# Kernel optimization log

Measured on AMD Instinct MI355X. Metric: run time of the kernel, lower is better.

## Reference

```python
import jax, jax.numpy as jnp
import numpy as np

N_NODES = 100000
N_EDGES = 2000000
FEAT = 4
H = 64
L = 3  # num_mp_layers
E = 2  # edge_types


def _p(key, shape, scale=0.05):
    return jax.random.normal(key, shape, dtype=jnp.float32) * scale


def setup_inputs() -> dict:
    key = jax.random.key(0)
    ks = jax.random.split(key, 24)
    inp = {
        "x": jax.random.normal(ks[0], (N_NODES, FEAT), dtype=jnp.float32),
        "node_type": jax.random.randint(ks[1], (N_NODES,), 0, 3),
        "edge_index": jax.random.randint(ks[2], (2, N_EDGES), 0, N_NODES),
        "edge_type": jax.random.randint(ks[3], (N_EDGES,), 0, E),
        # input_proj: Linear(4,64) + LayerNorm(64)
        "in_w": _p(ks[4], (FEAT, H)), "in_b": _p(ks[5], (H,)),
        "ln_g": jnp.ones((H,), jnp.float32), "ln_b": jnp.zeros((H,), jnp.float32),
        # per-layer, per-edge-type message MLPs: Linear(2H,H) -> ReLU -> Linear(H,H)
        "mlp_w1": _p(ks[6], (L, E, 2 * H, H)), "mlp_b1": _p(ks[7], (L, E, H)),
        "mlp_w2": _p(ks[8], (L, E, H, H)), "mlp_b2": _p(ks[9], (L, E, H)),
        # per-layer GRUCell(H,H): gates ordered [r, z, n] as in torch
        "gru_wi": _p(ks[10], (L, H, 3 * H)), "gru_wh": _p(ks[11], (L, H, 3 * H)),
        "gru_bi": _p(ks[12], (L, 3 * H)), "gru_bh": _p(ks[13], (L, 3 * H)),
        # readout: Linear(H,H) -> ReLU -> Linear(H,1)
        "ro_w1": _p(ks[14], (H, H)), "ro_b1": _p(ks[15], (H,)),
        "ro_w2": _p(ks[16], (H, 1)), "ro_b2": _p(ks[17], (1,)),
    }
    return inp


def _layernorm(h, g, b, eps=1e-5):
    mu = jnp.mean(h, axis=-1, keepdims=True)
    var = jnp.mean(jnp.square(h - mu), axis=-1, keepdims=True)
    return (h - mu) * jax.lax.rsqrt(var + eps) * g + b


def _forward(x, edge_index, edge_type, node_type,
             in_w, in_b, ln_g, ln_b,
             mlp_w1, mlp_b1, mlp_w2, mlp_b2,
             gru_wi, gru_wh, gru_bi, gru_bh,
             ro_w1, ro_b1, ro_w2, ro_b2):
    n = x.shape[0]
    # input projection (dropout is identity at inference)
    h = jax.nn.relu(_layernorm(x @ in_w + in_b, ln_g, ln_b))
    src, dst = edge_index[0], edge_index[1]
    for l in range(L):
        # gather -> concat: (M, 2H)
        mi = jnp.concatenate([h[src], h[dst]], axis=1)
        msg = jnp.zeros((mi.shape[0], H), dtype=h.dtype)
        for e in range(E):
            m = jax.nn.relu(mi @ mlp_w1[l, e] + mlp_b1[l, e]) @ mlp_w2[l, e] + mlp_b2[l, e]
            msg = msg + jnp.where((edge_type == e)[:, None], m, jnp.zeros((), h.dtype))
        # scatter_add over destination nodes
        agg = jax.ops.segment_sum(msg, dst, num_segments=n)
        # GRUCell(agg, h), torch gate order [r, z, n]
        gi = agg @ gru_wi[l] + gru_bi[l]
        gh = h @ gru_wh[l] + gru_bh[l]
        i_r, i_z, i_n = jnp.split(gi, 3, axis=-1)
        h_r, h_z, h_n = jnp.split(gh, 3, axis=-1)
        r = jax.nn.sigmoid(i_r + h_r)
        z = jax.nn.sigmoid(i_z + h_z)
        nn_ = jnp.tanh(i_n + r * h_n)
        h = (1.0 - z) * nn_ + z * h
    out = jax.nn.relu(h @ ro_w1 + ro_b1) @ ro_w2 + ro_b2  # (N, 1)
    # additive correction for data qubits (node_type==0); other nodes zeroed
    corr = jnp.where(node_type == 0, x[:, 0] + out[:, 0], jnp.zeros((), x.dtype))
    return corr


def reference(x, node_type, edge_index, edge_type,
              in_w, in_b, ln_g, ln_b,
              mlp_w1, mlp_b1, mlp_w2, mlp_b2,
              gru_wi, gru_wh, gru_bi, gru_bh,
              ro_w1, ro_b1, ro_w2, ro_b2):
    return _forward(x, edge_index, edge_type, node_type,
                    in_w, in_b, ln_g, ln_b,
                    mlp_w1, mlp_b1, mlp_w2, mlp_b2,
                    gru_wi, gru_wh, gru_bi, gru_bh,
                    ro_w1, ro_b1, ro_w2, ro_b2)
```

## Files before the change

kernel.cpp:

```cpp
#include <hip/hip_runtime.h>

typedef unsigned int u32;
typedef unsigned short u16;
typedef unsigned long long u64;

using short8 = __attribute__((ext_vector_type(8))) short;
using f32x4  = __attribute__((ext_vector_type(4))) float;

__device__ __forceinline__ u32 f2bf(float f) {
    u32 u = __float_as_uint(f);
    return (u + 0x7fffu + ((u >> 16) & 1u)) >> 16;
}
__device__ __forceinline__ u32 pk(float a, float b) {
    return f2bf(a) | (f2bf(b) << 16);
}
__device__ __forceinline__ u32 f2bf_fast(float f) {
    return (__float_as_uint(f) + 0x8000u) >> 16;
}
__device__ __forceinline__ u32 pk_fast(float a, float b) {
    return f2bf_fast(a) | (f2bf_fast(b) << 16);
}
__device__ __forceinline__ float bflo(u32 u) { return __uint_as_float(u << 16); }
__device__ __forceinline__ float bfhi(u32 u) { return __uint_as_float(u & 0xffff0000u); }
__device__ __forceinline__ float bfu(u16 u) { return __uint_as_float(((u32)u) << 16); }

union U8 { u32 u[4]; short8 v; };

__global__ void k_input_proj(const float* __restrict__ x, const float* __restrict__ in_w,
                             const float* __restrict__ in_b, const float* __restrict__ ln_g,
                             const float* __restrict__ ln_b, u16* __restrict__ hbf, int n_nodes) {
    const int lane = threadIdx.x & 63;
    const int node = blockIdx.x * 4 + (threadIdx.x >> 6);
    if (node >= n_nodes) return;
    float acc = in_b[lane];
#pragma unroll
    for (int k = 0; k < 4; ++k) acc = fmaf(x[node * 4 + k], in_w[k * 64 + lane], acc);
    float s = acc;
#pragma unroll
    for (int off = 32; off > 0; off >>= 1) s += __shfl_xor(s, off);
    float mu = s * (1.f / 64.f);
    float d = acc - mu;
    float vs = d * d;
#pragma unroll
    for (int off = 32; off > 0; off >>= 1) vs += __shfl_xor(vs, off);
    float inv = rsqrtf(vs * (1.f / 64.f) + 1e-5f);
    float hv = fmaxf(d * inv * ln_g[lane] + ln_b[lane], 0.f);
    hbf[(size_t)node * 64 + lane] = (u16)f2bf(hv);
}

__global__ void k_hist(const int* __restrict__ dst, const int* __restrict__ ety,
                       int* __restrict__ cnt, int M, int N) {
    int i = blockIdx.x * 256 + threadIdx.x;
    if (i < M) atomicAdd(&cnt[(ety[i] & 1) * N + dst[i]], 1);
}

__global__ void k_scan1(int* __restrict__ data, int* __restrict__ part, int N) {
    __shared__ int s[1024];
    const int t = threadIdx.x;
    const int i = blockIdx.x * 1024 + t;
    int v = (i < N) ? data[i] : 0;
    s[t] = v;
    __syncthreads();
#pragma unroll
    for (int d = 1; d < 1024; d <<= 1) {
        int x = (t >= d) ? s[t - d] : 0;
        __syncthreads();
        s[t] += x;
        __syncthreads();
    }
    if (i < N) data[i] = s[t] - v;
    if (t == 1023) part[blockIdx.x] = s[1023];
}

__global__ void k_scan2(int* __restrict__ part, int nb) {
    const int l = threadIdx.x & 63;
    int base = 0;
    for (int s = 0; s < nb; s += 64) {
        int i = s + l;
        int orig = (i < nb) ? part[i] : 0;
        int x = orig;
#pragma unroll
        for (int off = 1; off < 64; off <<= 1) {
            int t = __shfl_up(x, off);
            if (l >= off) x += t;
        }
        if (i < nb) part[i] = base + x - orig;
        base += __shfl(x, 63);
    }
}

__global__ void k_scan3(int* __restrict__ data, const int* __restrict__ part, int N,
                        int saveIdx, int* __restrict__ slot) {
    int i = blockIdx.x * 1024 + threadIdx.x;
    if (i < N) {
        int v = data[i] + part[blockIdx.x];
        data[i] = v;
        if (i == saveIdx) slot[0] = v;
    }
}

__global__ void k_filldst(const int* __restrict__ off, int* __restrict__ dstP,
                          int NB, int N, int M) {
    int b = blockIdx.x * 256 + threadIdx.x;
    if (b >= NB) return;
    int s = off[b];
    int e = (b + 1 < NB) ? off[b + 1] : M;
    int d = (b >= N) ? b - N : b;
    for (int p = s; p < e; ++p) dstP[p] = d;
}

__global__ void k_scatter(const int* __restrict__ src, const int* __restrict__ dst,
                          const int* __restrict__ ety, int* __restrict__ cursor,
                          int* __restrict__ srcP, int M, int N, int nd8) {
    const int g = blockIdx.x & 7;
    const int nb = gridDim.x >> 3;
    const int bi = blockIdx.x >> 3;
    for (int e = bi * 256 + threadIdx.x; e < M; e += nb * 256) {
        int d = dst[e];
        if (d / nd8 == g) {
            int t = ety[e] & 1;
            int pos = atomicAdd(&cursor[t * N + d], 1);
            srcP[pos] = src[e] & 0x3FFFFFFF;
        }
    }
}

__global__ __launch_bounds__(256, 2) void k_edge_mlp(
    const u16* __restrict__ hbf, const int* __restrict__ srcP, const int* __restrict__ dstP,
    const int* __restrict__ t0p, const float* __restrict__ w1, const float* __restrict__ b1,
    const float* __restrict__ w2, const float* __restrict__ b2,
    float* __restrict__ agg, int M) {
    __shared__ u16 sHid[4][4608];
    __shared__ u16 sMsg[4][4864];

    const int tid = threadIdx.x;
    const int l = tid & 63, wv = tid >> 6;
    const int l15 = l & 15, quad = l >> 4;
    const f32x4 vz = {0.f, 0.f, 0.f, 0.f};

    const int T0 = *t0p;
    const int half = gridDim.x >> 1;
    const int ty = (blockIdx.x >= half) ? 1 : 0;
    const int bi = ty ? (int)blockIdx.x - half : (int)blockIdx.x;

    const int n_tiles = (M + 63) >> 6;
    const int tlo = ty ? (T0 >> 6) : 0;
    const int thi = ty ? n_tiles : ((T0 + 63) >> 6);
    const int lo = ty ? T0 : 0;
    const int hi = ty ? M : T0;
    const int range = thi - tlo;
    const int per = (range + half - 1) / half;
    const int c0 = tlo + bi * per;
    const int c1 = min(c0 + per, thi);

    short8 Bf1[4][4], Bf2[2][4];
    float b1r[4], b2r[4];
#pragma unroll
    for (int ni = 0; ni < 4; ++ni) {
        const int c = ni * 16 + l15;
        b1r[ni] = b1[ty * 64 + c];
        b2r[ni] = b2[ty * 64 + c];
#pragma unroll
        for (int s = 0; s < 4; ++s) {
            U8 tmp;
            const float* wp = w1 + (size_t)ty * 8192 + (size_t)(s * 32 + quad * 8) * 64 + c;
#pragma unroll
            for (int jp = 0; jp < 4; ++jp) tmp.u[jp] = pk(wp[(2 * jp) * 64], wp[(2 * jp + 1) * 64]);
            Bf1[s][ni] = tmp.v;
        }
#pragma unroll
        for (int s = 0; s < 2; ++s) {
            U8 tmp;
            const float* wp = w2 + (size_t)ty * 4096 + (size_t)(s * 32 + quad * 8) * 64 + c;
#pragma unroll
            for (int jp = 0; jp < 4; ++jp) tmp.u[jp] = pk(wp[(2 * jp) * 64], wp[(2 * jp + 1) * 64]);
            Bf2[s][ni] = tmp.v;
        }
    }

    u16* hid = sHid[wv];
    u16* msg = sMsg[wv];

    int t = c0 + wv;
    int mdc = -1;
    int msn = 0, mdn = -1;
    short8 a1[4][4];
    if (t < c1) {
        int ec = min((t << 6) + l, M - 1);
        int ms = srcP[ec];
        mdc = dstP[ec];
#pragma unroll
        for (int mi = 0; mi < 4; ++mi) {
            int rs = __shfl(ms, mi * 16 + l15);
            int rd = __shfl(mdc, mi * 16 + l15);
#pragma unroll
            for (int s = 0; s < 4; ++s) {
                const int row = (s < 2) ? rs : rd;
                a1[mi][s] = *(const short8*)(hbf + (size_t)row * 64 + (s & 1) * 32 + quad * 8);
            }
        }
        int ecn = min(((t + 4) << 6) + l, M - 1);
        msn = srcP[ecn];
        mdn = dstP[ecn];
    }

    for (; t < c1; t += 4) {
        const int base = t << 6;
        const int ecf = min(((t + 8) << 6) + l, M - 1);
        const int msf = srcP[ecf];
        const int mdf = dstP[ecf];

#pragma unroll
        for (int mi = 0; mi < 4; ++mi) {
            f32x4 acc[4] = {vz, vz, vz, vz};
#pragma unroll
            for (int s = 0; s < 4; ++s)
#pragma unroll
                for (int ni = 0; ni < 4; ++ni)
                    acc[ni] = __builtin_amdgcn_mfma_f32_16x16x32_bf16(a1[mi][s], Bf1[s][ni], acc[ni], 0, 0, 0);
            {
                int rs = __shfl(msn, mi * 16 + l15);
                int rd = __shfl(mdn, mi * 16 + l15);
#pragma unroll
                for (int s = 0; s < 4; ++s) {
                    const int row = (s < 2) ? rs : rd;
                    a1[mi][s] = *(const short8*)(hbf + (size_t)row * 64 + (s & 1) * 32 + quad * 8);
                }
            }
#pragma unroll
            for (int ni = 0; ni < 4; ++ni) {
                const int c = ni * 16 + l15;
#pragma unroll
                for (int r = 0; r < 4; ++r) {
                    float hv = fmaxf(acc[ni][r] + b1r[ni], 0.f);
                    hid[(mi * 16 + quad * 4 + r) * 72 + c] = (u16)f2bf_fast(hv);
                }
            }
        }

#pragma unroll
        for (int mi = 0; mi < 4; ++mi) {
            short8 a2a = *(const short8*)(hid + (mi * 16 + l15) * 72 + quad * 8);
            short8 a2b = *(const short8*)(hid + (mi * 16 + l15) * 72 + 32 + quad * 8);
#pragma unroll
            for (int ni = 0; ni < 4; ++ni) {
                f32x4 tt = __builtin_amdgcn_mfma_f32_16x16x32_bf16(a2a, Bf2[0][ni], vz, 0, 0, 0);
                f32x4 m2 = __builtin_amdgcn_mfma_f32_16x16x32_bf16(a2b, Bf2[1][ni], tt, 0, 0, 0);
                const int c = ni * 16 + l15;
                const int e0 = mi * 16 + quad * 4;
                const float bb = b2r[ni];
                uint2 w;
                w.x = pk_fast(m2[0] + bb, m2[1] + bb);
                w.y = pk_fast(m2[2] + bb, m2[3] + bb);
                *(uint2*)(msg + c * 76 + e0) = w;
            }
        }

        {
            int eg = base + l;
            int dvz = (eg >= lo && eg < hi) ? mdc : -1;
            int dprev = __shfl_up(dvz, 1);
            u64 mask = __ballot((l == 0) || (dvz != dprev));
            float a = 0.f;
#pragma unroll
            for (int i = 0; i < 64; i += 4) {
                uint2 pr = *(const uint2*)(msg + l * 76 + i);
                float v0 = bflo(pr.x), v1 = bfhi(pr.x), v2 = bflo(pr.y), v3 = bfhi(pr.y);
#define RR_STEP(ii, vv)                                                         \
                a += (vv);                                                      \
                if ((ii) == 63 || ((mask >> ((ii) + 1)) & 1ull)) {              \
                    int dd = __builtin_amdgcn_readlane(dvz, (ii));              \
                    if (dd >= 0) unsafeAtomicAdd(agg + (size_t)dd * 64 + l, a); \
                    a = 0.f;                                                    \
                }
                RR_STEP(i, v0)
                RR_STEP(i + 1, v1)
                RR_STEP(i + 2, v2)
                RR_STEP(i + 3, v3)
#undef RR_STEP
            }
        }
        mdc = mdn;
        msn = msf;
        mdn = mdf;
    }
}

__global__ __launch_bounds__(256, 2) void k_gru_gemm(
    float* __restrict__ agg, u16* __restrict__ hbf,
    const float* __restrict__ wi, const float* __restrict__ wh,
    const float* __restrict__ bi, const float* __restrict__ bh, int n_nodes) {
    extern __shared__ u16 smem[];
    u16* sRZ = smem;
    u16* sIN = smem + 128 * 136;
    u16* sHN = sIN + 64 * 72;
    u16* sTR = sHN + 64 * 72;

    const int tid = threadIdx.x;
    const int l = tid & 63, wv = tid >> 6;
    const int l15 = l & 15, quad = l >> 4;
    const f32x4 vz = {0.f, 0.f, 0.f, 0.f};

    for (int u = tid; u < 128 * 64; u += 256) {
        int c = u & 127, k0 = (u >> 7) * 2;
        float v0 = (k0 < 64) ? wi[k0 * 192 + c] : wh[(k0 - 64) * 192 + c];
        float v1 = (k0 < 64) ? wi[(k0 + 1) * 192 + c] : wh[(k0 + 1 - 64) * 192 + c];
        *(u32*)(sRZ + c * 136 + k0) = pk(v0, v1);
    }
    for (int u = tid; u < 64 * 32; u += 256) {
        int c = u & 63, k0 = (u >> 6) * 2;
        *(u32*)(sIN + c * 72 + k0) = pk(wi[k0 * 192 + 128 + c], wi[(k0 + 1) * 192 + 128 + c]);
        *(u32*)(sHN + c * 72 + k0) = pk(wh[k0 * 192 + 128 + c], wh[(k0 + 1) * 192 + 128 + c]);
    }
    float bR[4], bZ[4], bI[4], bH[4];
#pragma unroll
    for (int nt = 0; nt < 4; ++nt) {
        int j = nt * 16 + l15;
        bR[nt] = bi[j] + bh[j];
        bZ[nt] = bi[64 + j] + bh[64 + j];
        bI[nt] = bi[128 + j];
        bH[nt] = bh[128 + j];
    }
    __syncthreads();

    u16* tr = sTR + wv * (16 * 72);
    const f32x4 z4 = {0.f, 0.f, 0.f, 0.f};
    const int n_tiles = (n_nodes + 15) >> 4;
    const int g = blockIdx.x & 7, jb = blockIdx.x >> 3, nbg = gridDim.x >> 3;
    const int per8 = (n_tiles + 7) >> 3;
    const int glo = g * per8, ghi = min(glo + per8, n_tiles);
    for (int tile = glo + jb * 4 + wv; tile < ghi; tile += nbg * 4) {
        const int nb = tile << 4;
        const int arow = nb + l15;
        const int rowc = (arow < n_nodes) ? arow : (n_nodes - 1);
        short8 aA[2], aH[2];
#pragma unroll
        for (int s = 0; s < 2; ++s) {
            const float* ap = agg + (size_t)rowc * 64 + s * 32 + quad * 8;
            U8 tt;
#pragma unroll
            for (int jp = 0; jp < 4; ++jp) tt.u[jp] = pk(ap[2 * jp], ap[2 * jp + 1]);
            aA[s] = tt.v;
            aH[s] = *(const short8*)(hbf + (size_t)rowc * 64 + s * 32 + quad * 8);
        }
        if (arow < n_nodes) {
#pragma unroll
            for (int s = 0; s < 2; ++s) {
                *(f32x4*)(agg + (size_t)rowc * 64 + s * 32 + quad * 8) = z4;
                *(f32x4*)(agg + (size_t)rowc * 64 + s * 32 + quad * 8 + 4) = z4;
            }
        }
        f32x4 D[16];
#pragma unroll
        for (int i = 0; i < 16; ++i) D[i] = vz;
#pragma unroll
        for (int nt = 0; nt < 8; ++nt) {
            const u16* bp = sRZ + (nt * 16 + l15) * 136 + quad * 8;
            D[nt] = __builtin_amdgcn_mfma_f32_16x16x32_bf16(aA[0], *(const short8*)bp, D[nt], 0, 0, 0);
            D[nt] = __builtin_amdgcn_mfma_f32_16x16x32_bf16(aA[1], *(const short8*)(bp + 32), D[nt], 0, 0, 0);
            D[nt] = __builtin_amdgcn_mfma_f32_16x16x32_bf16(aH[0], *(const short8*)(bp + 64), D[nt], 0, 0, 0);
            D[nt] = __builtin_amdgcn_mfma_f32_16x16x32_bf16(aH[1], *(const short8*)(bp + 96), D[nt], 0, 0, 0);
        }
#pragma unroll
        for (int nt = 0; nt < 4; ++nt) {
            const u16* ip = sIN + (nt * 16 + l15) * 72 + quad * 8;
            D[8 + nt] = __builtin_amdgcn_mfma_f32_16x16x32_bf16(aA[0], *(const short8*)ip, D[8 + nt], 0, 0, 0);
            D[8 + nt] = __builtin_amdgcn_mfma_f32_16x16x32_bf16(aA[1], *(const short8*)(ip + 32), D[8 + nt], 0, 0, 0);
            const u16* hp = sHN + (nt * 16 + l15) * 72 + quad * 8;
            D[12 + nt] = __builtin_amdgcn_mfma_f32_16x16x32_bf16(aH[0], *(const short8*)hp, D[12 + nt], 0, 0, 0);
            D[12 + nt] = __builtin_amdgcn_mfma_f32_16x16x32_bf16(aH[1], *(const short8*)(hp + 32), D[12 + nt], 0, 0, 0);
        }
#pragma unroll
        for (int nt = 0; nt < 4; ++nt) {
            const int j = nt * 16 + l15;
#pragma unroll
            for (int r = 0; r < 4; ++r) {
                const int nd = nb + quad * 4 + r;
                float rsv = D[nt][r] + bR[nt];
                float zsv = D[4 + nt][r] + bZ[nt];
                float inv = D[8 + nt][r] + bI[nt];
                float hnv = D[12 + nt][r] + bH[nt];
                float rr = 1.f / (1.f + __expf(-rsv));
                float zz = 1.f / (1.f + __expf(-zsv));
                float nn = tanhf(fmaf(rr, hnv, inv));
                float hv = (nd < n_nodes) ? bfu(hbf[(size_t)nd * 64 + j]) : 0.f;
                float nh = (1.f - zz) * nn + zz * hv;
                tr[(quad * 4 + r) * 72 + j] = (u16)f2bf(nh);
            }
        }
        {
            const int nd = nb + (l >> 2);
            if (nd < n_nodes) {
                const u16* sp = tr + (l >> 2) * 72 + (l & 3) * 16;
                uint4 va = *(const uint4*)sp;
                uint4 vb = *(const uint4*)(sp + 8);
                u16* dp = hbf + (size_t)nd * 64 + (l & 3) * 16;
                *(uint4*)dp = va;
                *(uint4*)(dp + 8) = vb;
            }
        }
    }
}

__global__ void k_readout(const u16* __restrict__ hbf, const float* __restrict__ x,
                          const int* __restrict__ node_type, const float* __restrict__ w1,
                          const float* __restrict__ b1, const float* __restrict__ w2,
                          const float* __restrict__ b2, float* __restrict__ out, int n_nodes) {
    const int lane = threadIdx.x & 63;
    const int node = blockIdx.x * 4 + (threadIdx.x >> 6);
    if (node >= n_nodes) return;
    float hv = bfu(hbf[(size_t)node * 64 + lane]);
    float acc = b1[lane];
    for (int k = 0; k < 64; ++k) acc = fmaf(__shfl(hv, k), w1[k * 64 + lane], acc);
    float t = fmaxf(acc, 0.f) * w2[lane];
#pragma unroll
    for (int off = 32; off > 0; off >>= 1) t += __shfl_xor(t, off);
    if (lane == 0) {
        float o = t + b2[0];
        out[node] = (node_type[node] == 0) ? (x[node * 4] + o) : 0.f;
    }
}

extern "C" void kernel_launch(void* const* d_in, const int* in_sizes, int n_in, void* d_out,
                              int out_size, void* d_ws, size_t ws_size, hipStream_t stream) {
    const float* x = (const float*)d_in[0];
    const int* node_type = (const int*)d_in[1];
    const int* edge_index = (const int*)d_in[2];
    const int* edge_type = (const int*)d_in[3];
    const float* in_w = (const float*)d_in[4];
    const float* in_b = (const float*)d_in[5];
    const float* ln_g = (const float*)d_in[6];
    const float* ln_b = (const float*)d_in[7];
    const float* mlp_w1 = (const float*)d_in[8];
    const float* mlp_b1 = (const float*)d_in[9];
    const float* mlp_w2 = (const float*)d_in[10];
    const float* mlp_b2 = (const float*)d_in[11];
    const float* gru_wi = (const float*)d_in[12];
    const float* gru_wh = (const float*)d_in[13];
    const float* gru_bi = (const float*)d_in[14];
    const float* gru_bh = (const float*)d_in[15];
    const float* ro_w1 = (const float*)d_in[16];
    const float* ro_b1 = (const float*)d_in[17];
    const float* ro_w2 = (const float*)d_in[18];
    const float* ro_b2 = (const float*)d_in[19];

    const int N = in_sizes[1];
    const int M = in_sizes[3];
    const int* src = edge_index;
    const int* dst = edge_index + M;

    char* wsb = (char*)d_ws;
    float* agg = (float*)wsb;
    u16* hbf = (u16*)(wsb + (size_t)N * 256);
    int* off = (int*)(wsb + (size_t)N * 384);
    int* part = (int*)(wsb + (size_t)N * 384 + (size_t)2 * N * 4);
    int* srcP = (int*)(wsb + (size_t)N * 384 + (size_t)2 * N * 4 + 4096);
    int* dstP = srcP + M;
    int* t0slot = part + 1000;

    const int NB = 2 * N;
    const int nb = (NB + 1023) / 1024;
    const int nd8 = (N + 7) / 8;

    hipMemsetAsync(off, 0, (size_t)NB * sizeof(int), stream);
    k_hist<<<(M + 255) / 256, 256, 0, stream>>>(dst, edge_type, off, M, N);
    k_scan1<<<nb, 1024, 0, stream>>>(off, part, NB);
    k_scan2<<<1, 64, 0, stream>>>(part, nb);
    k_scan3<<<nb, 1024, 0, stream>>>(off, part, NB, N, t0slot);
    k_filldst<<<(NB + 255) / 256, 256, 0, stream>>>(off, dstP, NB, N, M);
    k_scatter<<<2048, 256, 0, stream>>>(src, dst, edge_type, off, srcP, M, N, nd8);

    k_input_proj<<<(N + 3) / 4, 256, 0, stream>>>(x, in_w, in_b, ln_g, ln_b, hbf, N);
    hipMemsetAsync(agg, 0, (size_t)N * 64 * sizeof(float), stream);
    const size_t gruLds = (size_t)(128 * 136 + 64 * 72 + 64 * 72 + 4 * 16 * 72) * sizeof(u16);
    for (int l = 0; l < 3; ++l) {
        k_edge_mlp<<<1024, 256, 0, stream>>>(hbf, srcP, dstP, t0slot,
                                             mlp_w1 + (size_t)l * 2 * 128 * 64,
                                             mlp_b1 + (size_t)l * 2 * 64,
                                             mlp_w2 + (size_t)l * 2 * 64 * 64,
                                             mlp_b2 + (size_t)l * 2 * 64, agg, M);
        k_gru_gemm<<<1024, 256, gruLds, stream>>>(agg, hbf, gru_wi + (size_t)l * 64 * 192,
                                                  gru_wh + (size_t)l * 64 * 192,
                                                  gru_bi + (size_t)l * 192, gru_bh + (size_t)l * 192, N);
    }
    k_readout<<<(N + 3) / 4, 256, 0, stream>>>(hbf, x, node_type, ro_w1, ro_b1, ro_w2, ro_b2,
                                               (float*)d_out, N);
}
```

Measured before the change: 824.7 us.

## Accumulate messages in bf16 atomics, fuse readout into last GRU, precompute edge keys

The node aggregation buffer moves from fp32 to bf16 and is updated with packed bf16 global atomics. This halves the atomic and read traffic and removes the fp32-to-bf16 packing in the GRU kernel. The readout MLP now runs with MFMA inside the final GRU launch, and the agg zeroing moves into the input projection instead of a memset. The histogram pass also stores a combined type/dst key so the scatter pass can reuse it. In exchange, accumulating in bf16 loses precision over many atomic adds per node, which risks accuracy.

```diff
diff --git a/kernel.cpp b/kernel.cpp
--- a/kernel.cpp
+++ b/kernel.cpp
@@ -24,14 +24,21 @@
 __device__ __forceinline__ float bfhi(u32 u) { return __uint_as_float(u & 0xffff0000u); }
 __device__ __forceinline__ float bfu(u16 u) { return __uint_as_float(((u32)u) << 16); }
 
+__device__ __forceinline__ void atomic_add_bf16(u16* p, int c_odd, float v) {
+    u32 dat = f2bf(v) << (c_odd << 4);
+    asm volatile("global_atomic_pk_add_bf16 %0, %1, off" :: "v"((u64)p), "v"(dat) : "memory");
+}
+
 union U8 { u32 u[4]; short8 v; };
 
 __global__ void k_input_proj(const float* __restrict__ x, const float* __restrict__ in_w,
                              const float* __restrict__ in_b, const float* __restrict__ ln_g,
-                             const float* __restrict__ ln_b, u16* __restrict__ hbf, int n_nodes) {
+                             const float* __restrict__ ln_b, u16* __restrict__ hbf,
+                             u16* __restrict__ aggb, int n_nodes) {
     const int lane = threadIdx.x & 63;
     const int node = blockIdx.x * 4 + (threadIdx.x >> 6);
     if (node >= n_nodes) return;
+    aggb[(size_t)node * 64 + lane] = 0;
     float acc = in_b[lane];
 #pragma unroll
     for (int k = 0; k < 4; ++k) acc = fmaf(x[node * 4 + k], in_w[k * 64 + lane], acc);
@@ -49,9 +56,13 @@
 }
 
 __global__ void k_hist(const int* __restrict__ dst, const int* __restrict__ ety,
-                       int* __restrict__ cnt, int M, int N) {
+                       int* __restrict__ cnt, int* __restrict__ key, int M, int N) {
     int i = blockIdx.x * 256 + threadIdx.x;
-    if (i < M) atomicAdd(&cnt[(ety[i] & 1) * N + dst[i]], 1);
+    if (i < M) {
+        int k = (ety[i] & 1) * N + dst[i];
+        key[i] = k;
+        atomicAdd(&cnt[k], 1);
+    }
 }
 
 __global__ void k_scan1(int* __restrict__ data, int* __restrict__ part, int N) {
@@ -109,17 +120,17 @@
     for (int p = s; p < e; ++p) dstP[p] = d;
 }
 
-__global__ void k_scatter(const int* __restrict__ src, const int* __restrict__ dst,
-                          const int* __restrict__ ety, int* __restrict__ cursor,
-                          int* __restrict__ srcP, int M, int N, int nd8) {
+__global__ void k_scatter(const int* __restrict__ src, const int* __restrict__ key,
+                          int* __restrict__ cursor, int* __restrict__ srcP,
+                          int M, int N, int nd8) {
     const int g = blockIdx.x & 7;
     const int nb = gridDim.x >> 3;
     const int bi = blockIdx.x >> 3;
     for (int e = bi * 256 + threadIdx.x; e < M; e += nb * 256) {
-        int d = dst[e];
+        int k = key[e];
+        int d = (k >= N) ? k - N : k;
         if (d / nd8 == g) {
-            int t = ety[e] & 1;
-            int pos = atomicAdd(&cursor[t * N + d], 1);
+            int pos = atomicAdd(&cursor[k], 1);
             srcP[pos] = src[e] & 0x3FFFFFFF;
         }
     }
@@ -129,7 +140,7 @@
     const u16* __restrict__ hbf, const int* __restrict__ srcP, const int* __restrict__ dstP,
     const int* __restrict__ t0p, const float* __restrict__ w1, const float* __restrict__ b1,
     const float* __restrict__ w2, const float* __restrict__ b2,
-    float* __restrict__ agg, int M) {
+    u16* __restrict__ agg, int M) {
     __shared__ u16 sHid[4][4608];
     __shared__ u16 sMsg[4][4864];
 
@@ -266,12 +277,13 @@
             for (int i = 0; i < 64; i += 4) {
                 uint2 pr = *(const uint2*)(msg + l * 76 + i);
                 float v0 = bflo(pr.x), v1 = bfhi(pr.x), v2 = bflo(pr.y), v3 = bfhi(pr.y);
-#define RR_STEP(ii, vv)                                                         \
-                a += (vv);                                                      \
-                if ((ii) == 63 || ((mask >> ((ii) + 1)) & 1ull)) {              \
-                    int dd = __builtin_amdgcn_readlane(dvz, (ii));              \
-                    if (dd >= 0) unsafeAtomicAdd(agg + (size_t)dd * 64 + l, a); \
-                    a = 0.f;                                                    \
+#define RR_STEP(ii, vv)                                                              \
+                a += (vv);                                                           \
+                if ((ii) == 63 || ((mask >> ((ii) + 1)) & 1ull)) {                   \
+                    int dd = __builtin_amdgcn_readlane(dvz, (ii));                   \
+                    if (dd >= 0)                                                     \
+                        atomic_add_bf16(agg + (size_t)dd * 64 + (l & ~1), l & 1, a); \
+                    a = 0.f;                                                         \
                 }
                 RR_STEP(i, v0)
                 RR_STEP(i + 1, v1)
@@ -287,19 +299,24 @@
 }
 
 __global__ __launch_bounds__(256, 2) void k_gru_gemm(
-    float* __restrict__ agg, u16* __restrict__ hbf,
+    u16* __restrict__ aggb, u16* __restrict__ hbf,
     const float* __restrict__ wi, const float* __restrict__ wh,
-    const float* __restrict__ bi, const float* __restrict__ bh, int n_nodes) {
+    const float* __restrict__ bi, const float* __restrict__ bh, int n_nodes, int last,
+    const float* __restrict__ ro_w1, const float* __restrict__ ro_b1,
+    const float* __restrict__ ro_w2, const float* __restrict__ ro_b2,
+    const float* __restrict__ x, const int* __restrict__ node_type, float* __restrict__ out) {
     extern __shared__ u16 smem[];
     u16* sRZ = smem;
     u16* sIN = smem + 128 * 136;
     u16* sHN = sIN + 64 * 72;
     u16* sTR = sHN + 64 * 72;
+    u16* sRO = sTR + 4 * 16 * 72;
 
     const int tid = threadIdx.x;
     const int l = tid & 63, wv = tid >> 6;
     const int l15 = l & 15, quad = l >> 4;
     const f32x4 vz = {0.f, 0.f, 0.f, 0.f};
+    const short8 z8 = {0, 0, 0, 0, 0, 0, 0, 0};
 
     for (int u = tid; u < 128 * 64; u += 256) {
         int c = u & 127, k0 = (u >> 7) * 2;
@@ -311,8 +328,9 @@
         int c = u & 63, k0 = (u >> 6) * 2;
         *(u32*)(sIN + c * 72 + k0) = pk(wi[k0 * 192 + 128 + c], wi[(k0 + 1) * 192 + 128 + c]);
         *(u32*)(sHN + c * 72 + k0) = pk(wh[k0 * 192 + 128 + c], wh[(k0 + 1) * 192 + 128 + c]);
-    }
-    float bR[4], bZ[4], bI[4], bH[4];
+        *(u32*)(sRO + c * 72 + k0) = pk(ro_w1[k0 * 64 + c], ro_w1[(k0 + 1) * 64 + c]);
+    }
+    float bR[4], bZ[4], bI[4], bH[4], b1v[4], w2v[4];
 #pragma unroll
     for (int nt = 0; nt < 4; ++nt) {
         int j = nt * 16 + l15;
@@ -320,11 +338,13 @@
         bZ[nt] = bi[64 + j] + bh[64 + j];
         bI[nt] = bi[128 + j];
         bH[nt] = bh[128 + j];
-    }
+        b1v[nt] = ro_b1[j];
+        w2v[nt] = ro_w2[j];
+    }
+    const float b2s = ro_b2[0];
     __syncthreads();
 
     u16* tr = sTR + wv * (16 * 72);
-    const f32x4 z4 = {0.f, 0.f, 0.f, 0.f};
     const int n_tiles = (n_nodes + 15) >> 4;
     const int g = blockIdx.x & 7, jb = blockIdx.x >> 3, nbg = gridDim.x >> 3;
     const int per8 = (n_tiles + 7) >> 3;
@@ -336,19 +356,13 @@
         short8 aA[2], aH[2];
 #pragma unroll
         for (int s = 0; s < 2; ++s) {
-            const float* ap = agg + (size_t)rowc * 64 + s * 32 + quad * 8;
-            U8 tt;
-#pragma unroll
-            for (int jp = 0; jp < 4; ++jp) tt.u[jp] = pk(ap[2 * jp], ap[2 * jp + 1]);
-            aA[s] = tt.v;
+            aA[s] = *(const short8*)(aggb + (size_t)rowc * 64 + s * 32 + quad * 8);
             aH[s] = *(const short8*)(hbf + (size_t)rowc * 64 + s * 32 + quad * 8);
         }
-        if (arow < n_nodes) {
-#pragma unroll
-            for (int s = 0; s < 2; ++s) {
-                *(f32x4*)(agg + (size_t)rowc * 64 + s * 32 + quad * 8) = z4;
-                *(f32x4*)(agg + (size_t)rowc * 64 + s * 32 + quad * 8 + 4) = z4;
-            }
+        if (!last && arow < n_nodes) {
+#pragma unroll
+            for (int s = 0; s < 2; ++s)
+                *(short8*)(aggb + (size_t)rowc * 64 + s * 32 + quad * 8) = z8;
         }
         f32x4 D[16];
 #pragma unroll
@@ -399,25 +413,34 @@
                 *(uint4*)(dp + 8) = vb;
             }
         }
-    }
-}
-
-__global__ void k_readout(const u16* __restrict__ hbf, const float* __restrict__ x,
-                          const int* __restrict__ node_type, const float* __restrict__ w1,
-                          const float* __restrict__ b1, const float* __restrict__ w2,
-                          const float* __restrict__ b2, float* __restrict__ out, int n_nodes) {
-    const int lane = threadIdx.x & 63;
-    const int node = blockIdx.x * 4 + (threadIdx.x >> 6);
-    if (node >= n_nodes) return;
-    float hv = bfu(hbf[(size_t)node * 64 + lane]);
-    float acc = b1[lane];
-    for (int k = 0; k < 64; ++k) acc = fmaf(__shfl(hv, k), w1[k * 64 + lane], acc);
-    float t = fmaxf(acc, 0.f) * w2[lane];
-#pragma unroll
-    for (int off = 32; off > 0; off >>= 1) t += __shfl_xor(t, off);
-    if (lane == 0) {
-        float o = t + b2[0];
-        out[node] = (node_type[node] == 0) ? (x[node * 4] + o) : 0.f;
+        if (last) {
+            short8 ar0 = *(const short8*)(tr + l15 * 72 + quad * 8);
+            short8 ar1 = *(const short8*)(tr + l15 * 72 + 32 + quad * 8);
+            float p[4] = {0.f, 0.f, 0.f, 0.f};
+#pragma unroll
+            for (int nt = 0; nt < 4; ++nt) {
+                const u16* bp = sRO + (nt * 16 + l15) * 72 + quad * 8;
+                f32x4 acc = __builtin_amdgcn_mfma_f32_16x16x32_bf16(ar0, *(const short8*)bp, vz, 0, 0, 0);
+                acc = __builtin_amdgcn_mfma_f32_16x16x32_bf16(ar1, *(const short8*)(bp + 32), acc, 0, 0, 0);
+#pragma unroll
+                for (int r = 0; r < 4; ++r)
+                    p[r] += fmaxf(acc[r] + b1v[nt], 0.f) * w2v[nt];
+            }
+#pragma unroll
+            for (int off = 1; off < 16; off <<= 1)
+#pragma unroll
+                for (int r = 0; r < 4; ++r) p[r] += __shfl_xor(p[r], off);
+            if (l15 == 0) {
+#pragma unroll
+                for (int r = 0; r < 4; ++r) {
+                    const int nd = nb + quad * 4 + r;
+                    if (nd < n_nodes) {
+                        float o = p[r] + b2s;
+                        out[nd] = (node_type[nd] == 0) ? (x[nd * 4] + o) : 0.f;
+                    }
+                }
+            }
+        }
     }
 }
 
@@ -450,12 +473,13 @@
     const int* dst = edge_index + M;
 
     char* wsb = (char*)d_ws;
-    float* agg = (float*)wsb;
-    u16* hbf = (u16*)(wsb + (size_t)N * 256);
-    int* off = (int*)(wsb + (size_t)N * 384);
-    int* part = (int*)(wsb + (size_t)N * 384 + (size_t)2 * N * 4);
-    int* srcP = (int*)(wsb + (size_t)N * 384 + (size_t)2 * N * 4 + 4096);
+    u16* aggb = (u16*)wsb;
+    u16* hbf = (u16*)(wsb + (size_t)N * 128);
+    int* off = (int*)(wsb + (size_t)N * 256);
+    int* part = (int*)(wsb + (size_t)N * 256 + (size_t)2 * N * 4);
+    int* srcP = (int*)(wsb + (size_t)N * 256 + (size_t)2 * N * 4 + 4096);
     int* dstP = srcP + M;
+    int* key = dstP + M;
     int* t0slot = part + 1000;
 
     const int NB = 2 * N;
@@ -463,26 +487,27 @@
     const int nd8 = (N + 7) / 8;
 
     hipMemsetAsync(off, 0, (size_t)NB * sizeof(int), stream);
-    k_hist<<<(M + 255) / 256, 256, 0, stream>>>(dst, edge_type, off, M, N);
+    k_hist<<<(M + 255) / 256, 256, 0, stream>>>(dst, edge_type, off, key, M, N);
     k_scan1<<<nb, 1024, 0, stream>>>(off, part, NB);
     k_scan2<<<1, 64, 0, stream>>>(part, nb);
     k_scan3<<<nb, 1024, 0, stream>>>(off, part, NB, N, t0slot);
     k_filldst<<<(NB + 255) / 256, 256, 0, stream>>>(off, dstP, NB, N, M);
-    k_scatter<<<2048, 256, 0, stream>>>(src, dst, edge_type, off, srcP, M, N, nd8);
-
-    k_input_proj<<<(N + 3) / 4, 256, 0, stream>>>(x, in_w, in_b, ln_g, ln_b, hbf, N);
-    hipMemsetAsync(agg, 0, (size_t)N * 64 * sizeof(float), stream);
-    const size_t gruLds = (size_t)(128 * 136 + 64 * 72 + 64 * 72 + 4 * 16 * 72) * sizeof(u16);
+    k_scatter<<<2048, 256, 0, stream>>>(src, key, off, srcP, M, N, nd8);
+
+    k_input_proj<<<(N + 3) / 4, 256, 0, stream>>>(x, in_w, in_b, ln_g, ln_b, hbf, aggb, N);
+    const size_t gruLds =
+        (size_t)(128 * 136 + 64 * 72 + 64 * 72 + 4 * 16 * 72 + 64 * 72) * sizeof(u16);
     for (int l = 0; l < 3; ++l) {
         k_edge_mlp<<<1024, 256, 0, stream>>>(hbf, srcP, dstP, t0slot,
                                              mlp_w1 + (size_t)l * 2 * 128 * 64,
                                              mlp_b1 + (size_t)l * 2 * 64,
                                              mlp_w2 + (size_t)l * 2 * 64 * 64,
-                                             mlp_b2 + (size_t)l * 2 * 64, agg, M);
-        k_gru_gemm<<<1024, 256, gruLds, stream>>>(agg, hbf, gru_wi + (size_t)l * 64 * 192,
+                                             mlp_b2 + (size_t)l * 2 * 64, aggb, M);
+        k_gru_gemm<<<1024, 256, gruLds, stream>>>(aggb, hbf, gru_wi + (size_t)l * 64 * 192,
                                                   gru_wh + (size_t)l * 64 * 192,
-                                                  gru_bi + (size_t)l * 192, gru_bh + (size_t)l * 192, N);
-    }
-    k_readout<<<(N + 3) / 4, 256, 0, stream>>>(hbf, x, node_type, ro_w1, ro_b1, ro_w2, ro_b2,
-                                               (float*)d_out, N);
-}
+                                                  gru_bi + (size_t)l * 192, gru_bh + (size_t)l * 192,
+                                                  N, (l == 2) ? 1 : 0,
+                                                  ro_w1, ro_b1, ro_w2, ro_b2,
+                                                  x, node_type, (float*)d_out);
+    }
+}
```

Measured after the change: 1.492 ms. 80.9% more time.
